# Optimization experiments

Hardware: AMD Instinct MI355X
Metric: run time of the kernel (lower is better)

Reference implementation:

```python
import jax, jax.numpy as jnp
import numpy as np

B, N = 8192, 64
EPS = 1e-5
KARCHER_STEPS = 1


def _sym_apply(x, fn):
    # f(X) for symmetric X via eigendecomposition: V f(w) V^T
    w, v = jnp.linalg.eigh(x)
    return jnp.einsum('...ij,...j,...kj->...ik', v, fn(w), v)


def _logm(x):
    return _sym_apply(x, jnp.log)


def _expm(x):
    return _sym_apply(x, jnp.exp)


def sym_mat_pow(x, p):
    # X^p for SPD X, scalar (possibly traced) exponent p
    w, v = jnp.linalg.eigh(x)
    return jnp.einsum('...ij,...j,...kj->...ik', v, w ** p, v)


def _sqrt_and_invsqrt(m):
    # single eigh shared between m^{1/2} and m^{-1/2}
    w, v = jnp.linalg.eigh(m)
    sw = jnp.sqrt(w)
    s = jnp.einsum('...ij,...j,...kj->...ik', v, sw, v)
    si = jnp.einsum('...ij,...j,...kj->...ik', v, 1.0 / sw, v)
    return s, si


def karcher_flow(x, steps):
    # Frechet mean under AIRM via Karcher flow, init at arithmetic mean
    mean = x.mean(0)
    for _ in range(steps):
        s, si = _sqrt_and_invsqrt(mean)
        t = _logm(si @ x @ si).mean(0)  # mean tangent at current estimate
        mean = s @ _expm(t) @ s
    return mean


def batch_stats(x):
    mean = karcher_flow(x, KARCHER_STEPS)
    _, si = _sqrt_and_invsqrt(mean)
    logs = _logm(si @ x @ si)  # [B, n, n] tangent vectors at identity
    var = jnp.mean(jnp.sum(logs * logs, axis=(-2, -1)))  # mean squared AIRM distance
    return mean, jnp.sqrt(var)


def setup_inputs() -> dict:
    key = jax.random.key(0)
    k1, k2 = jax.random.split(key, 2)
    g = jax.random.normal(k1, (B, N, N), dtype=jnp.float32)
    x = g @ jnp.swapaxes(g, -1, -2) / N + 1e-3 * jnp.eye(N, dtype=jnp.float32)  # SPD batch
    h = jax.random.normal(k2, (N, N), dtype=jnp.float32)
    shift = h @ h.T / N + 0.1 * jnp.eye(N, dtype=jnp.float32)  # SPD shift parameter
    scale = jnp.ones((1,), dtype=jnp.float32)
    return {"x": x, "shift": shift, "scale": scale}


def reference(x, shift, scale):
    # batch stats are computed under no_grad in torch -> stop_gradient here
    mean, std = batch_stats(x)
    mean = jax.lax.stop_gradient(mean)
    std = jax.lax.stop_gradient(std)

    # parallel transport mean -> identity (whiten): mean^{-1/2} X mean^{-1/2}
    _, mi = _sqrt_and_invsqrt(mean)
    xw = mi @ x @ mi

    # scale by learnable scalar / batch std via matrix power
    p = (scale / (std + EPS))[0]
    y = sym_mat_pow(xw, p)

    # parallel transport identity -> shift: shift^{1/2} Y shift^{1/2}
    ss, _ = _sqrt_and_invsqrt(shift)
    return ss @ y @ ss
```

## Files before the change

### kernel.cpp

```cpp
#include <hip/hip_runtime.h>
#include <math.h>

#define ND 64
#define PAD 65
#define NN 4096
#define NB 8192

#define OFF_MEANPART ((size_t)0)
#define OFF_MEANA    ((size_t)131072)
#define OFF_S        ((size_t)135168)
#define OFF_SI       ((size_t)139264)
#define OFF_SS       ((size_t)143360)
#define OFF_TBAR     ((size_t)147456)
#define OFF_MI       ((size_t)151552)
#define OFF_P        ((size_t)155648)
#define OFF_VARPART  ((size_t)155712)
#define OFF_LAM      ((size_t)157760)
#define OFF_TPART    ((size_t)682048)

#define G2_BLOCKS 2048
#define G3_BLOCKS 2048

__device__ __forceinline__ float bperm_f(int pa, float x) {
  return __builtin_bit_cast(float,
      __builtin_amdgcn_ds_bpermute(pa, __builtin_bit_cast(int, x)));
}

__device__ __forceinline__ constexpr int skey(int row) { return (row + (row >> 4)) & 15; }
__device__ __forceinline__ int swz4(int row, int g) { return row * 64 + ((g ^ skey(row)) << 2); }
__device__ __forceinline__ int swzE(int row, int e) {
  return row * 64 + (((e >> 2) ^ skey(row)) << 2) + (e & 3);
}

__device__ float jacobi1s64(float (&w)[ND], int lane) {
  float a0 = 0.f, a1 = 0.f, a2 = 0.f, a3 = 0.f;
#pragma unroll
  for (int i = 0; i < ND; i += 4) {
    a0 = fmaf(w[i + 0], w[i + 0], a0);
    a1 = fmaf(w[i + 1], w[i + 1], a1);
    a2 = fmaf(w[i + 2], w[i + 2], a2);
    a3 = fmaf(w[i + 3], w[i + 3], a3);
  }
  float g = (a0 + a1) + (a2 + a3);

  for (int sweep = 0; sweep < 18; ++sweep) {
    bool any = false;
    for (int r = 1; r < ND; ++r) {
      int pa = (lane ^ r) << 2;
      float v[ND + 1];
#pragma unroll
      for (int i = 0; i <= ND; ++i) {
        float t = bperm_f(pa, (i < ND) ? w[i] : g);
        asm volatile("" : "+v"(t));
        v[i] = t;
      }
      float gv = v[ND];
      float b0 = 0.f, b1 = 0.f, b2 = 0.f, b3 = 0.f;
#pragma unroll
      for (int i = 0; i < ND; i += 4) {
        b0 = fmaf(w[i + 0], v[i + 0], b0);
        b1 = fmaf(w[i + 1], v[i + 1], b1);
        b2 = fmaf(w[i + 2], v[i + 2], b2);
        b3 = fmaf(w[i + 3], v[i + 3], b3);
      }
      float apq = (b0 + b1) + (b2 + b3);
      if (apq * apq > 4e-10f * g * gv) {
        int partner = lane ^ r;
        bool amP = lane < partner;
        float app = amP ? g : gv;
        float aqq = amP ? gv : g;
        float tau = (aqq - app) / (2.f * apq);
        float t = 1.f / (fabsf(tau) + sqrtf(1.f + tau * tau));
        t = (tau < 0.f) ? -t : t;
        float c = 1.f / sqrtf(1.f + t * t);
        float s = t * c;
        float s2v = amP ? -s : s;
#pragma unroll
        for (int i = 0; i < ND; ++i) w[i] = fmaf(s2v, v[i], c * w[i]);
        float d = t * apq;
        g = amP ? (g - d) : (g + d);
        any = true;
      }
    }
    if (!__any(any)) break;
  }
  a0 = a1 = a2 = a3 = 0.f;
#pragma unroll
  for (int i = 0; i < ND; i += 4) {
    a0 = fmaf(w[i + 0], w[i + 0], a0);
    a1 = fmaf(w[i + 1], w[i + 1], a1);
    a2 = fmaf(w[i + 2], w[i + 2], a2);
    a3 = fmaf(w[i + 3], w[i + 3], a3);
  }
  return (a0 + a1) + (a2 + a3);
}

__device__ __forceinline__ void congruence1(const float* __restrict__ xi,
                                            const float* __restrict__ q,
                                            float* __restrict__ Xb, int lane,
                                            float (&w)[ND]) {
#pragma unroll
  for (int k = 0; k < 16; ++k) {
    int flat = k * 256 + lane * 4;
    float4 rv = *(const float4*)(xi + flat);
    int a = flat >> 6;
    *(float4*)(Xb + swz4(a, lane & 15)) = rv;
  }
  __syncthreads();
  float B[ND];
#pragma unroll
  for (int r = 0; r < ND; ++r) B[r] = 0.f;
  const float* qc = q + lane * ND;
  for (int a = 0; a < ND; ++a) {
    float sa = qc[a];
#pragma unroll
    for (int g2 = 0; g2 < 16; ++g2) {
      float4 xa = *(const float4*)(Xb + swz4(a, g2));
      B[4 * g2 + 0] = fmaf(xa.x, sa, B[4 * g2 + 0]);
      B[4 * g2 + 1] = fmaf(xa.y, sa, B[4 * g2 + 1]);
      B[4 * g2 + 2] = fmaf(xa.z, sa, B[4 * g2 + 2]);
      B[4 * g2 + 3] = fmaf(xa.w, sa, B[4 * g2 + 3]);
    }
  }
  __syncthreads();
#pragma unroll
  for (int g2 = 0; g2 < 16; ++g2) {
    float4 b4 = make_float4(B[4 * g2 + 0], B[4 * g2 + 1], B[4 * g2 + 2], B[4 * g2 + 3]);
    *(float4*)(Xb + swz4(lane, g2)) = b4;
  }
#pragma unroll
  for (int r = 0; r < ND; ++r) w[r] = 0.f;
  for (int a = 0; a < ND; ++a) {
    float ba = Xb[swzE(lane, a)];
    const float* qr = q + a * ND;
#pragma unroll
    for (int r = 0; r < ND; ++r) w[r] = fmaf(qr[r], ba, w[r]);
  }
}

__device__ void jacobi2s(float (&A)[ND][PAD], float (&V)[ND][PAD], int tid) {
  __shared__ float cs_[32], sn_[32];
  __shared__ int   pp_[32], qq_[32];
  __shared__ int   rotcnt_;
  __shared__ float fro2_;
  __shared__ float red_[4];

  __syncthreads();
  float loc = 0.f;
  for (int e = tid; e < NN; e += 256) { float a = A[e >> 6][e & 63]; loc += a * a; }
  for (int o = 32; o; o >>= 1) loc += __shfl_down(loc, o);
  if ((tid & 63) == 0) red_[tid >> 6] = loc;
  __syncthreads();
  if (tid == 0) fro2_ = red_[0] + red_[1] + red_[2] + red_[3];
  __syncthreads();
  float fro2 = fro2_;

  for (int sweep = 0; sweep < 20; ++sweep) {
    if (tid == 0) rotcnt_ = 0;
    __syncthreads();
    for (int r = 0; r < 63; ++r) {
      if (tid < 32) {
        int p, q;
        if (tid == 0) { p = 63; q = r; }
        else { p = (r + tid) % 63; q = (r + 63 - tid) % 63; }
        if (p > q) { int t0 = p; p = q; q = t0; }
        pp_[tid] = p; qq_[tid] = q;
        float app = A[p][p], aqq = A[q][q], apq = A[p][q];
        float thr = fmaxf(1e-12f * fabsf(app * aqq), 1e-14f * fro2);
        float c = 1.f, s = 0.f;
        if (apq * apq > thr) {
          float tau = (aqq - app) / (2.f * apq);
          float t = 1.f / (fabsf(tau) + sqrtf(1.f + tau * tau));
          t = (tau < 0.f) ? -t : t;
          c = 1.f / sqrtf(1.f + t * t);
          s = t * c;
          atomicAdd(&rotcnt_, 1);
        }
        cs_[tid] = c; sn_[tid] = s;
      }
      __syncthreads();
      for (int t = tid; t < 2048; t += 256) {
        int k = t >> 6, j = t & 63;
        int p = pp_[k], q = qq_[k]; float c = cs_[k], s = sn_[k];
        float ap = A[p][j], aq = A[q][j];
        A[p][j] = c * ap - s * aq;
        A[q][j] = s * ap + c * aq;
      }
      __syncthreads();
      for (int t = tid; t < 4096; t += 256) {
        int k = (t >> 6) & 31, j = t & 63;
        int p = pp_[k], q = qq_[k]; float c = cs_[k], s = sn_[k];
        if (t < 2048) {
          float ap = A[j][p], aq = A[j][q];
          A[j][p] = c * ap - s * aq;
          A[j][q] = s * ap + c * aq;
        } else {
          float vp = V[j][p], vq = V[j][q];
          V[j][p] = c * vp - s * vq;
          V[j][q] = s * vp + c * vq;
        }
      }
      __syncthreads();
    }
    int rc = rotcnt_;
    __syncthreads();
    if (rc == 0) break;
  }
}

__device__ void recon_write(const float (&V)[ND][PAD], const float* f, float* g,
                            int c, int wq) {
  float acc[16];
#pragma unroll
  for (int k = 0; k < 16; ++k) acc[k] = 0.f;
  for (int j = 0; j < ND; ++j) {
    float m = f[j] * V[c][j];
#pragma unroll
    for (int k = 0; k < 16; ++k) acc[k] = fmaf(V[wq + 4 * k][j], m, acc[k]);
  }
#pragma unroll
  for (int k = 0; k < 16; ++k) g[(wq + 4 * k) * ND + c] = acc[k];
}

__global__ __launch_bounds__(256) void k_mean_part(const float* __restrict__ x,
                                                   float* __restrict__ part) {
  int e = blockIdx.x * 256 + threadIdx.x;
  int chunk = blockIdx.y;
  const float* px = x + (size_t)chunk * 256 * NN + e;
  float s = 0.f;
  for (int i = 0; i < 256; ++i) s += px[(size_t)i * NN];
  part[(size_t)chunk * NN + e] = s;
}

__global__ __launch_bounds__(256) void k_mean_final(const float* __restrict__ part,
                                                    float* __restrict__ meanA) {
  int e = blockIdx.x * 256 + threadIdx.x;
  float s = 0.f;
  for (int c = 0; c < 32; ++c) s += part[(size_t)c * NN + e];
  meanA[e] = s * (1.f / (float)NB);
}

__global__ __launch_bounds__(256) void k_prep1(const float* __restrict__ meanA,
                                               const float* __restrict__ shift,
                                               float* __restrict__ s_out,
                                               float* __restrict__ si_out,
                                               float* __restrict__ ss_out) {
  __shared__ float A[ND][PAD], V[ND][PAD];
  __shared__ float f1[ND], f2[ND];
  int tid = threadIdx.x;
  const float* src = (blockIdx.x == 0) ? meanA : shift;
  for (int e = tid; e < NN; e += 256) A[e >> 6][e & 63] = src[e];
  for (int e = tid; e < NN; e += 256) V[e >> 6][e & 63] = ((e >> 6) == (e & 63)) ? 1.f : 0.f;
  jacobi2s(A, V, tid);
  if (tid < ND) {
    float wv = fmaxf(A[tid][tid], 1e-30f);
    f1[tid] = sqrtf(wv);
    f2[tid] = 1.f / sqrtf(wv);
  }
  __syncthreads();
  int c = tid & 63, wq = tid >> 6;
  if (blockIdx.x == 0) {
    recon_write(V, f1, s_out, c, wq);
    recon_write(V, f2, si_out, c, wq);
  } else {
    recon_write(V, f1, ss_out, c, wq);
  }
}

__global__ __launch_bounds__(64, 1) void k_stage2(const float* __restrict__ x,
                                                  const float* __restrict__ si,
                                                  float* __restrict__ tPart,
                                                  int G2) {
  __shared__ float Xb[4096];
  int lane = threadIdx.x;

  float tacc[ND];
#pragma unroll
  for (int i = 0; i < ND; ++i) tacc[i] = 0.f;

  for (int i = blockIdx.x; i < NB; i += G2) {
    __syncthreads();
    float w[ND];
    congruence1(x + (size_t)i * NN, si, Xb, lane, w);
    float s2 = jacobi1s64(w, lane);
    float sig = sqrtf(fmaxf(s2, 1e-38f));
    float inv = 1.f / sig;
    float lg = logf(sig);
#pragma unroll
    for (int g2 = 0; g2 < 16; ++g2) {
      float4 u4 = make_float4(w[4 * g2 + 0] * inv, w[4 * g2 + 1] * inv,
                              w[4 * g2 + 2] * inv, w[4 * g2 + 3] * inv);
      *(float4*)(Xb + swz4(lane, g2)) = u4;
    }
    __syncthreads();
    for (int j = 0; j < ND; ++j) {
      float lwj = __shfl(lg, j);
      float uj = Xb[swzE(j, lane)];
      float m = lwj * uj;
#pragma unroll
      for (int g2 = 0; g2 < 16; ++g2) {
        float4 u4 = *(const float4*)(Xb + swz4(j, g2));
        tacc[4 * g2 + 0] = fmaf(u4.x, m, tacc[4 * g2 + 0]);
        tacc[4 * g2 + 1] = fmaf(u4.y, m, tacc[4 * g2 + 1]);
        tacc[4 * g2 + 2] = fmaf(u4.z, m, tacc[4 * g2 + 2]);
        tacc[4 * g2 + 3] = fmaf(u4.w, m, tacc[4 * g2 + 3]);
      }
    }
  }
#pragma unroll
  for (int r = 0; r < ND; ++r)
    tPart[(size_t)blockIdx.x * NN + r * ND + lane] = tacc[r];
}

__global__ __launch_bounds__(256) void k_reduce_t(const float* __restrict__ tPart,
                                                  float* __restrict__ tbar, int nw) {
  int e = blockIdx.x * 256 + threadIdx.x;
  float s = 0.f;
  for (int b = 0; b < nw; ++b) s += tPart[(size_t)b * NN + e];
  tbar[e] = s * (1.f / (float)NB);
}

__global__ __launch_bounds__(256) void k_prep2(const float* __restrict__ tbar,
                                               const float* __restrict__ s_g,
                                               float* __restrict__ mi_out) {
  __shared__ float A[ND][PAD], V[ND][PAD];
  __shared__ float f1[ND];
  int tid = threadIdx.x;
  int c = tid & 63, wq = tid >> 6;
  for (int e = tid; e < NN; e += 256) A[e >> 6][e & 63] = tbar[e];
  for (int e = tid; e < NN; e += 256) V[e >> 6][e & 63] = ((e >> 6) == (e & 63)) ? 1.f : 0.f;
  jacobi2s(A, V, tid);
  if (tid < ND) f1[tid] = expf(A[tid][tid]);
  __syncthreads();
  {
    float acc[16];
#pragma unroll
    for (int k = 0; k < 16; ++k) acc[k] = 0.f;
    for (int j = 0; j < ND; ++j) {
      float m = f1[j] * V[c][j];
#pragma unroll
      for (int k = 0; k < 16; ++k) acc[k] = fmaf(V[wq + 4 * k][j], m, acc[k]);
    }
    __syncthreads();
#pragma unroll
    for (int k = 0; k < 16; ++k) A[wq + 4 * k][c] = acc[k];
  }
  __syncthreads();
  {
    float acc[16];
#pragma unroll
    for (int k = 0; k < 16; ++k) acc[k] = 0.f;
    for (int a = 0; a < ND; ++a) {
      float ea = A[a][c];
#pragma unroll
      for (int k = 0; k < 16; ++k) acc[k] = fmaf(s_g[(wq + 4 * k) * ND + a], ea, acc[k]);
    }
    __syncthreads();
#pragma unroll
    for (int k = 0; k < 16; ++k) V[wq + 4 * k][c] = acc[k];
  }
  __syncthreads();
  {
    float acc[16];
#pragma unroll
    for (int k = 0; k < 16; ++k) acc[k] = 0.f;
    for (int a = 0; a < ND; ++a) {
      float sa = s_g[a * ND + c];
#pragma unroll
      for (int k = 0; k < 16; ++k) acc[k] = fmaf(V[wq + 4 * k][a], sa, acc[k]);
    }
    __syncthreads();
#pragma unroll
    for (int k = 0; k < 16; ++k) A[wq + 4 * k][c] = acc[k];
  }
  __syncthreads();
  for (int e = tid; e < NN; e += 256) V[e >> 6][e & 63] = ((e >> 6) == (e & 63)) ? 1.f : 0.f;
  jacobi2s(A, V, tid);
  if (tid < ND) f1[tid] = 1.f / sqrtf(fmaxf(A[tid][tid], 1e-30f));
  __syncthreads();
  recon_write(V, f1, mi_out, c, wq);
}

__global__ __launch_bounds__(64, 1) void k_stage3(const float* __restrict__ x,
                                                  const float* __restrict__ mi,
                                                  const float* __restrict__ ss,
                                                  float* __restrict__ aout,
                                                  float* __restrict__ lam,
                                                  float* __restrict__ varPart,
                                                  int G3) {
  __shared__ float Xb[4096];
  int lane = threadIdx.x;
  float varacc = 0.f;

  for (int i = blockIdx.x; i < NB; i += G3) {
    __syncthreads();
    float w[ND];
    congruence1(x + (size_t)i * NN, mi, Xb, lane, w);
    float s2 = jacobi1s64(w, lane);
    float sig = sqrtf(fmaxf(s2, 1e-38f));
    float inv = 1.f / sig;
    lam[(size_t)i * ND + lane] = sig;
    float lg = logf(sig);
    varacc = fmaf(lg, lg, varacc);
#pragma unroll
    for (int g2 = 0; g2 < 16; ++g2) {
      float4 u4 = make_float4(w[4 * g2 + 0] * inv, w[4 * g2 + 1] * inv,
                              w[4 * g2 + 2] * inv, w[4 * g2 + 3] * inv);
      *(float4*)(Xb + swz4(lane, g2)) = u4;
    }
    float acc[ND];
#pragma unroll
    for (int r = 0; r < ND; ++r) acc[r] = 0.f;
    for (int a = 0; a < ND; ++a) {
      float ua = Xb[swzE(lane, a)];
      const float* ssr = ss + a * ND;
#pragma unroll
      for (int r = 0; r < ND; ++r) acc[r] = fmaf(ssr[r], ua, acc[r]);
    }
#pragma unroll
    for (int r = 0; r < ND; ++r)
      aout[(size_t)i * NN + r * ND + lane] = acc[r];
  }
  for (int o = 32; o; o >>= 1) varacc += __shfl_down(varacc, o);
  if (lane == 0) varPart[blockIdx.x] = varacc;
}

__global__ __launch_bounds__(64) void k_pfinal(const float* __restrict__ varPart,
                                               const float* __restrict__ scale,
                                               float* __restrict__ pout, int n) {
  int tid = threadIdx.x;
  float s = 0.f;
  for (int i = tid; i < n; i += 64) s += varPart[i];
  for (int o = 32; o; o >>= 1) s += __shfl_down(s, o);
  if (tid == 0) {
    float var = s * (1.f / (float)NB);
    float sd = sqrtf(var);
    pout[0] = scale[0] / (sd + 1e-5f);
  }
}

__global__ __launch_bounds__(256) void k_stage5(const float* __restrict__ ain,
                                                const float* __restrict__ lam,
                                                const float* __restrict__ pws,
                                                float* __restrict__ out) {
  __shared__ float Ab[ND][PAD];
  __shared__ float lp[ND];
  int tid = threadIdx.x;
  int i = blockIdx.x;
  for (int e = tid; e < NN; e += 256) Ab[e >> 6][e & 63] = ain[(size_t)i * NN + e];
  if (tid < ND) {
    float p = pws[0];
    lp[tid] = powf(lam[(size_t)i * ND + tid], p);
  }
  __syncthreads();
  int c = tid & 63, wq = tid >> 6;
  float acc[16];
#pragma unroll
  for (int k = 0; k < 16; ++k) acc[k] = 0.f;
  for (int j = 0; j < ND; ++j) {
    float m = lp[j] * Ab[c][j];
#pragma unroll
    for (int k = 0; k < 16; ++k) acc[k] = fmaf(Ab[wq + 4 * k][j], m, acc[k]);
  }
#pragma unroll
  for (int k = 0; k < 16; ++k)
    out[(size_t)i * NN + (wq + 4 * k) * ND + c] = acc[k];
}

extern "C" void kernel_launch(void* const* d_in, const int* in_sizes, int n_in,
                              void* d_out, int out_size, void* d_ws, size_t ws_size,
                              hipStream_t stream) {
  const float* x     = (const float*)d_in[0];
  const float* shift = (const float*)d_in[1];
  const float* scale = (const float*)d_in[2];
  float* out = (float*)d_out;
  float* ws  = (float*)d_ws;
  (void)in_sizes; (void)n_in; (void)out_size;

  size_t wsf = ws_size / 4;
  int G2 = G2_BLOCKS;
  if (OFF_TPART + (size_t)G2 * NN > wsf) {
    size_t avail = (wsf > OFF_TPART) ? (wsf - OFF_TPART) / NN : 1;
    if (avail < 1) avail = 1;
    if (avail < (size_t)G2) G2 = (int)avail;
  }

  k_mean_part<<<dim3(16, 32), 256, 0, stream>>>(x, ws + OFF_MEANPART);
  k_mean_final<<<16, 256, 0, stream>>>(ws + OFF_MEANPART, ws + OFF_MEANA);
  k_prep1<<<2, 256, 0, stream>>>(ws + OFF_MEANA, shift, ws + OFF_S, ws + OFF_SI,
                                 ws + OFF_SS);
  k_stage2<<<G2, 64, 0, stream>>>(x, ws + OFF_SI, ws + OFF_TPART, G2);
  k_reduce_t<<<16, 256, 0, stream>>>(ws + OFF_TPART, ws + OFF_TBAR, G2);
  k_prep2<<<1, 256, 0, stream>>>(ws + OFF_TBAR, ws + OFF_S, ws + OFF_MI);
  k_stage3<<<G3_BLOCKS, 64, 0, stream>>>(x, ws + OFF_MI, ws + OFF_SS, out,
                                         ws + OFF_LAM, ws + OFF_VARPART, G3_BLOCKS);
  k_pfinal<<<1, 64, 0, stream>>>(ws + OFF_VARPART, scale, ws + OFF_P, G3_BLOCKS);
  k_stage5<<<8192, 256, 0, stream>>>(out, ws + OFF_LAM, ws + OFF_P, out);
}
```

Measured before the change: 16.29 ms.

## Split Jacobi kernels from tangent and shift GEMMs, halve LDS for occupancy

The per-matrix one-sided Jacobi kernels shrink their shared buffer to 2048 floats by staging X in two halves, and raise launch bounds to allow three waves per CU. The tangent accumulation and the shift congruence move out of the register-heavy Jacobi kernels: eigenvectors and log-eigenvalues go to global memory, and separate 256-thread kernels do the rank-weighted outer products and the ss multiply. The aim is better latency hiding on the Jacobi path. The cost is an extra full-batch write and read of U through the output buffer, plus another kernel launch.

```diff
diff --git a/kernel.cpp b/kernel.cpp
--- a/kernel.cpp
+++ b/kernel.cpp
@@ -24,12 +24,6 @@
 __device__ __forceinline__ float bperm_f(int pa, float x) {
   return __builtin_bit_cast(float,
       __builtin_amdgcn_ds_bpermute(pa, __builtin_bit_cast(int, x)));
-}
-
-__device__ __forceinline__ constexpr int skey(int row) { return (row + (row >> 4)) & 15; }
-__device__ __forceinline__ int swz4(int row, int g) { return row * 64 + ((g ^ skey(row)) << 2); }
-__device__ __forceinline__ int swzE(int row, int e) {
-  return row * 64 + (((e >> 2) ^ skey(row)) << 2) + (e & 3);
 }
 
 __device__ float jacobi1s64(float (&w)[ND], int lane) {
@@ -95,46 +89,48 @@
   return (a0 + a1) + (a2 + a3);
 }
 
-__device__ __forceinline__ void congruence1(const float* __restrict__ xi,
+__device__ __forceinline__ void congruence2(const float* __restrict__ xi,
                                             const float* __restrict__ q,
-                                            float* __restrict__ Xb, int lane,
+                                            float* __restrict__ XL, int lane,
                                             float (&w)[ND]) {
-#pragma unroll
-  for (int k = 0; k < 16; ++k) {
-    int flat = k * 256 + lane * 4;
-    float4 rv = *(const float4*)(xi + flat);
-    int a = flat >> 6;
-    *(float4*)(Xb + swz4(a, lane & 15)) = rv;
-  }
-  __syncthreads();
   float B[ND];
 #pragma unroll
-  for (int r = 0; r < ND; ++r) B[r] = 0.f;
+  for (int i = 0; i < ND; ++i) B[i] = 0.f;
+
   const float* qc = q + lane * ND;
-  for (int a = 0; a < ND; ++a) {
-    float sa = qc[a];
-#pragma unroll
-    for (int g2 = 0; g2 < 16; ++g2) {
-      float4 xa = *(const float4*)(Xb + swz4(a, g2));
-      B[4 * g2 + 0] = fmaf(xa.x, sa, B[4 * g2 + 0]);
-      B[4 * g2 + 1] = fmaf(xa.y, sa, B[4 * g2 + 1]);
-      B[4 * g2 + 2] = fmaf(xa.z, sa, B[4 * g2 + 2]);
-      B[4 * g2 + 3] = fmaf(xa.w, sa, B[4 * g2 + 3]);
-    }
-  }
-  __syncthreads();
-#pragma unroll
-  for (int g2 = 0; g2 < 16; ++g2) {
-    float4 b4 = make_float4(B[4 * g2 + 0], B[4 * g2 + 1], B[4 * g2 + 2], B[4 * g2 + 3]);
-    *(float4*)(Xb + swz4(lane, g2)) = b4;
-  }
-#pragma unroll
-  for (int r = 0; r < ND; ++r) w[r] = 0.f;
-  for (int a = 0; a < ND; ++a) {
-    float ba = Xb[swzE(lane, a)];
-    const float* qr = q + a * ND;
-#pragma unroll
-    for (int r = 0; r < ND; ++r) w[r] = fmaf(qr[r], ba, w[r]);
+  for (int p = 0; p < 2; ++p) {
+#pragma unroll
+    for (int k = 0; k < 8; ++k) {
+      int m = k * 64 + lane;
+      float4 rv = ((const float4*)(xi + p * 2048))[m];
+      int phys = m ^ ((m >> 4) & 7);
+      ((float4*)XL)[phys] = rv;
+    }
+    for (int a0 = 0; a0 < 32; ++a0) {
+      int a = p * 32 + a0;
+      float sa = qc[a];
+      int base = a0 * 16, sw = a0 & 7;
+#pragma unroll
+      for (int k = 0; k < 16; ++k) {
+        const float4 c4 = ((const float4*)XL)[base + (k ^ sw)];
+        B[4 * k + 0] = fmaf(c4.x, sa, B[4 * k + 0]);
+        B[4 * k + 1] = fmaf(c4.y, sa, B[4 * k + 1]);
+        B[4 * k + 2] = fmaf(c4.z, sa, B[4 * k + 2]);
+        B[4 * k + 3] = fmaf(c4.w, sa, B[4 * k + 3]);
+      }
+    }
+  }
+#pragma unroll
+  for (int i = 0; i < ND; ++i) w[i] = 0.f;
+  for (int h = 0; h < 2; ++h) {
+#pragma unroll
+    for (int j = 0; j < 32; ++j) XL[j * ND + lane] = B[h * 32 + j];
+    for (int a0 = 0; a0 < 32; ++a0) {
+      float ba = XL[a0 * ND + lane];
+      const float* qr = q + (h * 32 + a0) * ND;
+#pragma unroll
+      for (int r = 0; r < ND; ++r) w[r] = fmaf(qr[r], ba, w[r]);
+    }
   }
 }
 
@@ -267,49 +263,55 @@
   }
 }
 
-__global__ __launch_bounds__(64, 1) void k_stage2(const float* __restrict__ x,
-                                                  const float* __restrict__ si,
-                                                  float* __restrict__ tPart,
-                                                  int G2) {
-  __shared__ float Xb[4096];
+__global__ __launch_bounds__(64, 3) void k_stage2jac(const float* __restrict__ x,
+                                                     const float* __restrict__ si,
+                                                     float* __restrict__ uout,
+                                                     float* __restrict__ lgout,
+                                                     int G2) {
+  __shared__ float XL[2048];
   int lane = threadIdx.x;
-
-  float tacc[ND];
-#pragma unroll
-  for (int i = 0; i < ND; ++i) tacc[i] = 0.f;
-
   for (int i = blockIdx.x; i < NB; i += G2) {
-    __syncthreads();
     float w[ND];
-    congruence1(x + (size_t)i * NN, si, Xb, lane, w);
+    congruence2(x + (size_t)i * NN, si, XL, lane, w);
     float s2 = jacobi1s64(w, lane);
     float sig = sqrtf(fmaxf(s2, 1e-38f));
     float inv = 1.f / sig;
-    float lg = logf(sig);
+    lgout[(size_t)i * ND + lane] = logf(sig);
 #pragma unroll
     for (int g2 = 0; g2 < 16; ++g2) {
       float4 u4 = make_float4(w[4 * g2 + 0] * inv, w[4 * g2 + 1] * inv,
                               w[4 * g2 + 2] * inv, w[4 * g2 + 3] * inv);
-      *(float4*)(Xb + swz4(lane, g2)) = u4;
-    }
+      *(float4*)(uout + (size_t)i * NN + lane * ND + g2 * 4) = u4;
+    }
+  }
+}
+
+__global__ __launch_bounds__(256) void k_tangent(const float* __restrict__ uin,
+                                                 const float* __restrict__ lg,
+                                                 float* __restrict__ tPart,
+                                                 int G2) {
+  __shared__ float Ut[ND][PAD];
+  __shared__ float lw[ND];
+  int tid = threadIdx.x;
+  int c = tid & 63, wq = tid >> 6;
+  float acc[16];
+#pragma unroll
+  for (int k = 0; k < 16; ++k) acc[k] = 0.f;
+
+  for (int i = blockIdx.x; i < NB; i += G2) {
+    __syncthreads();
+    for (int e = tid; e < NN; e += 256) Ut[e >> 6][e & 63] = uin[(size_t)i * NN + e];
+    if (tid < ND) lw[tid] = lg[(size_t)i * ND + tid];
     __syncthreads();
     for (int j = 0; j < ND; ++j) {
-      float lwj = __shfl(lg, j);
-      float uj = Xb[swzE(j, lane)];
-      float m = lwj * uj;
-#pragma unroll
-      for (int g2 = 0; g2 < 16; ++g2) {
-        float4 u4 = *(const float4*)(Xb + swz4(j, g2));
-        tacc[4 * g2 + 0] = fmaf(u4.x, m, tacc[4 * g2 + 0]);
-        tacc[4 * g2 + 1] = fmaf(u4.y, m, tacc[4 * g2 + 1]);
-        tacc[4 * g2 + 2] = fmaf(u4.z, m, tacc[4 * g2 + 2]);
-        tacc[4 * g2 + 3] = fmaf(u4.w, m, tacc[4 * g2 + 3]);
-      }
-    }
-  }
-#pragma unroll
-  for (int r = 0; r < ND; ++r)
-    tPart[(size_t)blockIdx.x * NN + r * ND + lane] = tacc[r];
+      float m = lw[j] * Ut[j][c];
+#pragma unroll
+      for (int k = 0; k < 16; ++k) acc[k] = fmaf(Ut[j][wq + 4 * k], m, acc[k]);
+    }
+  }
+#pragma unroll
+  for (int k = 0; k < 16; ++k)
+    tPart[(size_t)blockIdx.x * NN + (wq + 4 * k) * ND + c] = acc[k];
 }
 
 __global__ __launch_bounds__(256) void k_reduce_t(const float* __restrict__ tPart,
@@ -381,21 +383,18 @@
   recon_write(V, f1, mi_out, c, wq);
 }
 
-__global__ __launch_bounds__(64, 1) void k_stage3(const float* __restrict__ x,
-                                                  const float* __restrict__ mi,
-                                                  const float* __restrict__ ss,
-                                                  float* __restrict__ aout,
-                                                  float* __restrict__ lam,
-                                                  float* __restrict__ varPart,
-                                                  int G3) {
-  __shared__ float Xb[4096];
+__global__ __launch_bounds__(64, 3) void k_stage3jac(const float* __restrict__ x,
+                                                     const float* __restrict__ mi,
+                                                     float* __restrict__ uout,
+                                                     float* __restrict__ lam,
+                                                     float* __restrict__ varPart,
+                                                     int G3) {
+  __shared__ float XL[2048];
   int lane = threadIdx.x;
   float varacc = 0.f;
-
   for (int i = blockIdx.x; i < NB; i += G3) {
-    __syncthreads();
     float w[ND];
-    congruence1(x + (size_t)i * NN, mi, Xb, lane, w);
+    congruence2(x + (size_t)i * NN, mi, XL, lane, w);
     float s2 = jacobi1s64(w, lane);
     float sig = sqrtf(fmaxf(s2, 1e-38f));
     float inv = 1.f / sig;
@@ -406,20 +405,8 @@
     for (int g2 = 0; g2 < 16; ++g2) {
       float4 u4 = make_float4(w[4 * g2 + 0] * inv, w[4 * g2 + 1] * inv,
                               w[4 * g2 + 2] * inv, w[4 * g2 + 3] * inv);
-      *(float4*)(Xb + swz4(lane, g2)) = u4;
-    }
-    float acc[ND];
-#pragma unroll
-    for (int r = 0; r < ND; ++r) acc[r] = 0.f;
-    for (int a = 0; a < ND; ++a) {
-      float ua = Xb[swzE(lane, a)];
-      const float* ssr = ss + a * ND;
-#pragma unroll
-      for (int r = 0; r < ND; ++r) acc[r] = fmaf(ssr[r], ua, acc[r]);
-    }
-#pragma unroll
-    for (int r = 0; r < ND; ++r)
-      aout[(size_t)i * NN + r * ND + lane] = acc[r];
+      *(float4*)(uout + (size_t)i * NN + lane * ND + g2 * 4) = u4;
+    }
   }
   for (int o = 32; o; o >>= 1) varacc += __shfl_down(varacc, o);
   if (lane == 0) varPart[blockIdx.x] = varacc;
@@ -439,32 +426,43 @@
   }
 }
 
-__global__ __launch_bounds__(256) void k_stage5(const float* __restrict__ ain,
+__global__ __launch_bounds__(256) void k_stage5(const float* __restrict__ uin,
+                                                const float* __restrict__ ss,
                                                 const float* __restrict__ lam,
                                                 const float* __restrict__ pws,
                                                 float* __restrict__ out) {
-  __shared__ float Ab[ND][PAD];
+  __shared__ float Ut[ND][PAD];
+  __shared__ float A2[ND][PAD];
   __shared__ float lp[ND];
   int tid = threadIdx.x;
   int i = blockIdx.x;
-  for (int e = tid; e < NN; e += 256) Ab[e >> 6][e & 63] = ain[(size_t)i * NN + e];
-  if (tid < ND) {
-    float p = pws[0];
-    lp[tid] = powf(lam[(size_t)i * ND + tid], p);
-  }
+  for (int e = tid; e < NN; e += 256) Ut[e >> 6][e & 63] = uin[(size_t)i * NN + e];
+  if (tid < ND) lp[tid] = powf(lam[(size_t)i * ND + tid], pws[0]);
   __syncthreads();
   int c = tid & 63, wq = tid >> 6;
   float acc[16];
 #pragma unroll
   for (int k = 0; k < 16; ++k) acc[k] = 0.f;
+  for (int a = 0; a < ND; ++a) {
+    float ua = Ut[c][a];
+    const float* ssr = ss + a * ND;
+#pragma unroll
+    for (int k = 0; k < 16; ++k) acc[k] = fmaf(ssr[wq + 4 * k], ua, acc[k]);
+  }
+#pragma unroll
+  for (int k = 0; k < 16; ++k) A2[wq + 4 * k][c] = acc[k];
+  __syncthreads();
+  float o2[16];
+#pragma unroll
+  for (int k = 0; k < 16; ++k) o2[k] = 0.f;
   for (int j = 0; j < ND; ++j) {
-    float m = lp[j] * Ab[c][j];
-#pragma unroll
-    for (int k = 0; k < 16; ++k) acc[k] = fmaf(Ab[wq + 4 * k][j], m, acc[k]);
+    float m = lp[j] * A2[c][j];
+#pragma unroll
+    for (int k = 0; k < 16; ++k) o2[k] = fmaf(A2[wq + 4 * k][j], m, o2[k]);
   }
 #pragma unroll
   for (int k = 0; k < 16; ++k)
-    out[(size_t)i * NN + (wq + 4 * k) * ND + c] = acc[k];
+    out[(size_t)i * NN + (wq + 4 * k) * ND + c] = o2[k];
 }
 
 extern "C" void kernel_launch(void* const* d_in, const int* in_sizes, int n_in,
@@ -489,11 +487,13 @@
   k_mean_final<<<16, 256, 0, stream>>>(ws + OFF_MEANPART, ws + OFF_MEANA);
   k_prep1<<<2, 256, 0, stream>>>(ws + OFF_MEANA, shift, ws + OFF_S, ws + OFF_SI,
                                  ws + OFF_SS);
-  k_stage2<<<G2, 64, 0, stream>>>(x, ws + OFF_SI, ws + OFF_TPART, G2);
+  k_stage2jac<<<G2, 64, 0, stream>>>(x, ws + OFF_SI, out, ws + OFF_LAM, G2);
+  k_tangent<<<G2, 256, 0, stream>>>(out, ws + OFF_LAM, ws + OFF_TPART, G2);
   k_reduce_t<<<16, 256, 0, stream>>>(ws + OFF_TPART, ws + OFF_TBAR, G2);
   k_prep2<<<1, 256, 0, stream>>>(ws + OFF_TBAR, ws + OFF_S, ws + OFF_MI);
-  k_stage3<<<G3_BLOCKS, 64, 0, stream>>>(x, ws + OFF_MI, ws + OFF_SS, out,
-                                         ws + OFF_LAM, ws + OFF_VARPART, G3_BLOCKS);
+  k_stage3jac<<<G3_BLOCKS, 64, 0, stream>>>(x, ws + OFF_MI, out, ws + OFF_LAM,
+                                            ws + OFF_VARPART, G3_BLOCKS);
   k_pfinal<<<1, 64, 0, stream>>>(ws + OFF_VARPART, scale, ws + OFF_P, G3_BLOCKS);
-  k_stage5<<<8192, 256, 0, stream>>>(out, ws + OFF_LAM, ws + OFF_P, out);
-}
+  k_stage5<<<8192, 256, 0, stream>>>(out, ws + OFF_SS, ws + OFF_LAM, ws + OFF_P,
+                                     out);
+}
```

Measured after the change: 17.01 ms. 4.4% more time.
